# Kernel optimization log

Hardware: AMD Instinct MI355X
Metric: run time of the kernel (lower is better)

## Reference

```python
import jax, jax.numpy as jnp
import numpy as np
from jax import lax

DN = ('NCHW', 'OIHW', 'NCHW')


def _cell(x, h, c, W, b):
    # x,h,c: [B,C,H,W]; W: [4C,2C,3,3]; b: [4C]
    combined = jnp.concatenate([x, h], axis=1)
    y = lax.conv_general_dilated(combined, W, (1, 1), 'SAME', dimension_numbers=DN)
    y = y + b[None, :, None, None]
    cc_i, cc_f, cc_o, cc_g = jnp.split(y, 4, axis=1)
    c_new = jax.nn.sigmoid(cc_f) * c + jax.nn.sigmoid(cc_i) * jnp.tanh(cc_g)
    h_new = jax.nn.sigmoid(cc_o) * jnp.tanh(c_new)
    return h_new, c_new


def _run_level(feats, mask, Wf, bf, Wb, bb):
    # feats: [T,B,C,H,W]; mask: [T,B] int
    zeros = jnp.zeros(feats.shape[1:], feats.dtype)

    def step(carry, xs):
        hf, cf, hb, cb = carry
        x, m = xs
        keep = (m > 0)[:, None, None, None]  # [B,1,1,1]
        nhf, ncf = _cell(x, hf, cf, Wf, bf)
        nhb, ncb = _cell(x, hb, cb, Wb, bb)
        hf = jnp.where(keep, nhf, hf)
        cf = jnp.where(keep, ncf, cf)
        hb = jnp.where(keep, nhb, hb)
        cb = jnp.where(keep, ncb, cb)
        return (hf, cf, hb, cb), None

    (hf, cf, hb, cb), _ = lax.scan(step, (zeros, zeros, zeros, zeros), (feats, mask))
    return (hf + hb) / 2.0


def _make_conv(key, C):
    fan_in = 2 * C * 9
    W = jax.random.normal(key, (4 * C, 2 * C, 3, 3), jnp.float32) / np.sqrt(fan_in)
    b = jnp.zeros((4 * C,), jnp.float32)
    return W, b


def setup_inputs() -> dict:
    key = jax.random.key(0)
    ks = jax.random.split(key, 8)
    feat0 = jax.random.normal(ks[0], (16, 8, 64, 64, 64), jnp.float32)
    feat1 = jax.random.normal(ks[1], (16, 8, 128, 32, 32), jnp.float32)
    mask = jax.random.randint(ks[2], (16, 8), 0, 2, jnp.int32)
    W_fwd0, b_fwd0 = _make_conv(ks[3], 64)
    W_bwd0, b_bwd0 = _make_conv(ks[4], 64)
    W_fwd1, b_fwd1 = _make_conv(ks[5], 128)
    W_bwd1, b_bwd1 = _make_conv(ks[6], 128)
    return {
        'feat0': feat0, 'feat1': feat1, 'mask': mask,
        'W_fwd0': W_fwd0, 'b_fwd0': b_fwd0, 'W_bwd0': W_bwd0, 'b_bwd0': b_bwd0,
        'W_fwd1': W_fwd1, 'b_fwd1': b_fwd1, 'W_bwd1': W_bwd1, 'b_bwd1': b_bwd1,
    }


def reference(feat0, feat1, mask, W_fwd0, b_fwd0, W_bwd0, b_bwd0,
              W_fwd1, b_fwd1, W_bwd1, b_bwd1):
    out0 = _run_level(feat0, mask, W_fwd0, b_fwd0, W_bwd0, b_bwd0)
    out1 = _run_level(feat1, mask, W_fwd1, b_fwd1, W_bwd1, b_bwd1)
    return (out0, out1)
```

## Files before the change

kernel.cpp:

```cpp
#include <hip/hip_runtime.h>

typedef __bf16 bf16x8 __attribute__((ext_vector_type(8)));
typedef float f32x4 __attribute__((ext_vector_type(4)));

__device__ __forceinline__ float sigmoidf_fast(float x) {
  return 1.f / (1.f + __expf(-x));
}
__device__ __forceinline__ float tanhf_fast(float x) {
  float e = __expf(2.f * x);
  return 1.f - 2.f / (e + 1.f);
}
__device__ __forceinline__ unsigned pack2(float a, float b) {
  unsigned short ua = __builtin_bit_cast(unsigned short, (__bf16)a);
  unsigned short ub = __builtin_bit_cast(unsigned short, (__bf16)b);
  return (unsigned)ua | ((unsigned)ub << 16);
}

__global__ void transpose_w_kernel(const float* __restrict__ Wsrc,
                                   __bf16* __restrict__ Wt, int C4, int C2) {
  int idx = blockIdx.x * 256 + threadIdx.x;
  int total = C4 * C2 * 9;
  if (idx >= total) return;
  int SLT = C2 >> 5;
  int j = idx & 7;
  int e = idx >> 3;
  int oc = e % C4; e /= C4;
  int q = e & 3;   e >>= 2;
  int sl = e % SLT;
  int tap = e / SLT;
  int ci = sl * 32 + q * 8 + j;
  Wt[idx] = (__bf16)Wsrc[(oc * C2 + ci) * 9 + tap];
}

__global__ void build_wbuf_kernel(const int* __restrict__ mask,
                                  int* __restrict__ wbuf) {
  int b = threadIdx.x;
  if (b >= 8) return;
  int m = 0;
  for (int t = 0; t < 16; ++t) {
    int w = 0;
    if (mask[t * 8 + b] > 0) { w = m & 1; ++m; }
    wbuf[t * 8 + b] = w;
  }
  wbuf[128 + b] = (m > 0) ? ((m - 1) & 1) : 0;
}

__global__ void combine_kernel(const float* __restrict__ h,
                               const int* __restrict__ fin,
                               float* __restrict__ out, int n, int chw,
                               size_t SZ) {
  int idx = blockIdx.x * 256 + threadIdx.x;
  if (idx >= n) return;
  int b = idx / chw;
  const float* hb = h + (size_t)fin[b] * 2 * SZ;
  out[idx] = (hb[idx] + hb[SZ + idx]) * 0.5f;
}

constexpr int SMEM_BYTES = 107712;

template <int C, int H, int W, int OROWS>
__device__ __forceinline__ void convlstm_block(
    char* smem, const float* __restrict__ x_t,
    const __bf16* __restrict__ Wt, const float* __restrict__ bias,
    const float* __restrict__ h_in, float* __restrict__ h_out,
    float* __restrict__ c_st, int d, int b, int y0, int cs)
{
  constexpr int Bz = 8, C2 = 2 * C, C4 = 4 * C;
  constexpr int COLS = W + 2, C2p = C2 + 8, IMR = OROWS + 2;
  constexpr int PLANE = H * W, CHW = C * PLANE;
  constexpr int SLT = C2 / 32;
  constexpr int LSLT = (SLT == 4) ? 2 : 3;
  constexpr int NSL = 9 * SLT;
  constexpr int ASL = 32 * C4;
  constexpr int CTPR = (W / 16) < 4 ? (W / 16) : 4;
  constexpr int RPG = OROWS / 2;
  constexpr int IMG_ITERS = (C2 / 4) * IMR * W / 512;

  __bf16* sT = (__bf16*)smem;

  const int tid = threadIdx.x;
  const float* hin_b = h_in + (size_t)(d * Bz + b) * CHW;
  float* hout_b = h_out + (size_t)(d * Bz + b) * CHW;
  const __bf16* Wtd = Wt + (size_t)d * (9 * C4 * C2);

  const int lane = tid & 63, wv = tid >> 6;
  const int rg = wv >> 2, wvr = wv & 3;
  const int n = lane & 15, q = lane >> 4;

  const __bf16* Ap = Wtd + (size_t)(q * C4 + cs * 64 + wvr * 16 + n) * 8;

  uint4 A0[4], A1[4];
  auto loadA = [&](int sl, uint4 (&A)[4]) {
    const __bf16* p = Ap + (size_t)sl * ASL;
#pragma unroll
    for (int g = 0; g < 4; ++g)
      A[g] = *reinterpret_cast<const uint4*>(p + g * (C * 8));
  };

  loadA(0, A0);
  loadA(1, A1);

  const float* x_b = x_t + (size_t)b * CHW;
#pragma unroll
  for (int it = 0; it < IMG_ITERS; ++it) {
    int u = it * 512 + tid;
    int x = u % W;
    int t2 = u / W;
    int rr = t2 % IMR, ci4 = t2 / IMR;
    int yy = y0 + rr - 1;
    uint2 pv; pv.x = 0u; pv.y = 0u;
    if (yy >= 0 && yy < H) {
      int ci = ci4 * 4;
      const float* s0 = ((ci < C) ? (x_b + (size_t)ci * PLANE)
                                  : (hin_b + (size_t)(ci - C) * PLANE)) +
                        (size_t)yy * W + x;
      float f0 = s0[0];
      float f1 = s0[PLANE];
      float f2 = s0[2 * PLANE];
      float f3 = s0[3 * PLANE];
      pv.x = pack2(f0, f1);
      pv.y = pack2(f2, f3);
    }
    *reinterpret_cast<uint2*>(&sT[(rr * COLS + x + 1) * C2p + ci4 * 4]) = pv;
  }
  for (int u = tid; u < (C2 / 4) * IMR * 2; u += 512) {
    int ci4 = u / (IMR * 2);
    int rem = u % (IMR * 2);
    int rr = rem >> 1;
    int slot = (rem & 1) ? (W + 1) : 0;
    uint2 z; z.x = 0u; z.y = 0u;
    *reinterpret_cast<uint2*>(&sT[(rr * COLS + slot) * C2p + ci4 * 4]) = z;
  }
  __syncthreads();

  f32x4 acc[4][4];
  f32x4 zero = {0.f, 0.f, 0.f, 0.f};
#pragma unroll
  for (int g = 0; g < 4; ++g)
#pragma unroll
    for (int nt = 0; nt < 4; ++nt) acc[g][nt] = zero;

  auto loadB = [&](int sl, bf16x8 (&Bv)[4]) {
    int tap = sl >> LSLT;
    int ci0 = (sl & (SLT - 1)) * 32;
    int ky = (tap * 11) >> 5;
    int kx = tap - 3 * ky;
#pragma unroll
    for (int nt = 0; nt < 4; ++nt) {
      int row = rg * RPG + nt / CTPR + ky;
      int slot = (nt % CTPR) * 16 + n + kx;
      Bv[nt] = *reinterpret_cast<const bf16x8*>(
          &sT[(row * COLS + slot) * C2p + ci0 + q * 8]);
    }
  };
  auto mfmaAll = [&](uint4 (&A)[4], bf16x8 (&Bv)[4]) {
#pragma unroll
    for (int g = 0; g < 4; ++g) {
      bf16x8 a = __builtin_bit_cast(bf16x8, A[g]);
#pragma unroll
      for (int nt = 0; nt < 4; ++nt)
        acc[g][nt] = __builtin_amdgcn_mfma_f32_16x16x32_bf16(
            a, Bv[nt], acc[g][nt], 0, 0, 0);
    }
  };

  bf16x8 B0[4], B1[4];
  loadB(0, B0);
  loadB(1, B1);
  for (int sl = 0; sl < NSL - 2; sl += 2) {
    mfmaAll(A0, B0);
    loadA(sl + 2, A0);
    loadB(sl + 2, B0);
    mfmaAll(A1, B1);
    loadA(sl + 3, A1);
    loadB(sl + 3, B1);
  }
  mfmaAll(A0, B0);
  mfmaAll(A1, B1);

  float* c_b = c_st + (size_t)(d * Bz + b) * CHW;
#pragma unroll
  for (int r = 0; r < 4; ++r) {
    const int cg = cs * 64 + wvr * 16 + q * 4 + r;
    const float bi = bias[0 * C + cg];
    const float bff = bias[1 * C + cg];
    const float bo = bias[2 * C + cg];
    const float bg = bias[3 * C + cg];
#pragma unroll
    for (int nt = 0; nt < 4; ++nt) {
      const int y = y0 + rg * RPG + nt / CTPR;
      const int x = (nt % CTPR) * 16 + n;
      const size_t off = (size_t)cg * PLANE + (size_t)y * W + x;
      const float vi = acc[0][nt][r] + bi;
      const float vf = acc[1][nt][r] + bff;
      const float vo = acc[2][nt][r] + bo;
      const float vg = acc[3][nt][r] + bg;
      const float cn = sigmoidf_fast(vf) * c_b[off] + sigmoidf_fast(vi) * tanhf_fast(vg);
      c_b[off] = cn;
      hout_b[off] = sigmoidf_fast(vo) * tanhf_fast(cn);
    }
  }
}

__global__ __launch_bounds__(512, 2)
void step_kernel(const float* __restrict__ x0, const float* __restrict__ x1,
                 const int* __restrict__ mask_t, const int* __restrict__ wbuf_t,
                 int* __restrict__ counter,
                 const __bf16* __restrict__ Wt0, const __bf16* __restrict__ Wt1,
                 const float* __restrict__ bf0, const float* __restrict__ bb0,
                 const float* __restrict__ bf1, const float* __restrict__ bb1,
                 float* __restrict__ h0, float* __restrict__ c0,
                 float* __restrict__ h1, float* __restrict__ c1)
{
  __shared__ __align__(16) char smem[SMEM_BYTES];
  __shared__ int s_pop;
  constexpr size_t SZ0 = (size_t)8 * 64 * 64 * 64;
  constexpr size_t SZ1 = (size_t)8 * 128 * 32 * 32;

  for (;;) {
    __syncthreads();
    if (threadIdx.x == 0) s_pop = atomicAdd(counter, 1);
    __syncthreads();
    const int idx = s_pop;
    if (idx >= 768) return;

    if (idx < 256) {
      int grp = idx >> 6;
      int d = grp >> 1, cs = grp & 1;
      int r = idx & 63;
      int b = r & 7, yb = r >> 3;
      if (mask_t[b] <= 0) continue;
      int w = wbuf_t[b];
      convlstm_block<128, 32, 32, 4>(smem, x1, Wt1,
          d == 0 ? bf1 : bb1,
          h1 + (size_t)(1 - w) * 2 * SZ1, h1 + (size_t)w * 2 * SZ1,
          c1, d, b, yb * 4, cs);
    } else {
      int j = idx - 256;
      int d = j >> 8;
      int r = j & 255;
      int b = r & 7, yb = r >> 3;
      if (mask_t[b] <= 0) continue;
      int w = wbuf_t[b];
      convlstm_block<64, 64, 64, 2>(smem, x0, Wt0,
          d == 0 ? bf0 : bb0,
          h0 + (size_t)(1 - w) * 2 * SZ0, h0 + (size_t)w * 2 * SZ0,
          c0, d, b, yb * 2, 0);
    }
  }
}

extern "C" void kernel_launch(void* const* d_in, const int* in_sizes, int n_in,
                              void* d_out, int out_size, void* d_ws, size_t ws_size,
                              hipStream_t stream) {
  const float* feat0 = (const float*)d_in[0];
  const float* feat1 = (const float*)d_in[1];
  const int* mask = (const int*)d_in[2];
  const float* Wf0 = (const float*)d_in[3];
  const float* bf0 = (const float*)d_in[4];
  const float* Wb0 = (const float*)d_in[5];
  const float* bb0 = (const float*)d_in[6];
  const float* Wf1 = (const float*)d_in[7];
  const float* bf1 = (const float*)d_in[8];
  const float* Wb1 = (const float*)d_in[9];
  const float* bb1 = (const float*)d_in[10];

  const int T = 16;
  const size_t SZ0 = (size_t)8 * 64 * 64 * 64;
  const size_t SZ1 = (size_t)8 * 128 * 32 * 32;
  const size_t WT0 = (size_t)9 * 256 * 128;
  const size_t WT1 = (size_t)9 * 512 * 256;

  char* p = (char*)d_ws;
  __bf16* Wt0 = (__bf16*)p; p += 2 * WT0 * sizeof(__bf16);
  __bf16* Wt1 = (__bf16*)p; p += 2 * WT1 * sizeof(__bf16);
  float* h0 = (float*)p;    p += 4 * SZ0 * sizeof(float);
  float* h1 = (float*)p;    p += 4 * SZ1 * sizeof(float);
  float* c0 = (float*)p;    p += 2 * SZ0 * sizeof(float);
  float* c1 = (float*)p;    p += 2 * SZ1 * sizeof(float);
  int* wbuf = (int*)p;      p += 256 * sizeof(int);
  int* counters = (int*)p;  p += 16 * sizeof(int);

  hipMemsetAsync(h0, 0, 4 * SZ0 * sizeof(float), stream);
  hipMemsetAsync(h1, 0, 4 * SZ1 * sizeof(float), stream);
  hipMemsetAsync(c0, 0, 2 * SZ0 * sizeof(float), stream);
  hipMemsetAsync(c1, 0, 2 * SZ1 * sizeof(float), stream);
  hipMemsetAsync(counters, 0, 16 * sizeof(int), stream);

  transpose_w_kernel<<<((int)WT0 + 255) / 256, 256, 0, stream>>>(Wf0, Wt0, 256, 128);
  transpose_w_kernel<<<((int)WT0 + 255) / 256, 256, 0, stream>>>(Wb0, Wt0 + WT0, 256, 128);
  transpose_w_kernel<<<((int)WT1 + 255) / 256, 256, 0, stream>>>(Wf1, Wt1, 512, 256);
  transpose_w_kernel<<<((int)WT1 + 255) / 256, 256, 0, stream>>>(Wb1, Wt1 + WT1, 512, 256);
  build_wbuf_kernel<<<1, 8, 0, stream>>>(mask, wbuf);

  for (int t = 0; t < T; ++t) {
    step_kernel<<<256, 512, 0, stream>>>(
        feat0 + (size_t)t * SZ0, feat1 + (size_t)t * SZ1,
        mask + t * 8, wbuf + t * 8, counters + t,
        Wt0, Wt1, bf0, bb0, bf1, bb1,
        h0, c0, h1, c1);
  }

  float* out = (float*)d_out;
  combine_kernel<<<((int)SZ0 + 255) / 256, 256, 0, stream>>>(
      h0, wbuf + 128, out, (int)SZ0, 64 * 64 * 64, SZ0);
  combine_kernel<<<((int)SZ1 + 255) / 256, 256, 0, stream>>>(
      h1, wbuf + 128, out + SZ0, (int)SZ1, 128 * 32 * 32, SZ1);
}
```

Baseline: 1.297 ms.

## Double per-block output tile and interleave half-tile B loads with MFMAs

```diff
diff --git a/kernel.cpp b/kernel.cpp
--- a/kernel.cpp
+++ b/kernel.cpp
@@ -58,22 +58,24 @@
 
 constexpr int SMEM_BYTES = 107712;
 
-template <int C, int H, int W, int OROWS>
+template <int C, int H, int W, int WAVES_M>
 __device__ __forceinline__ void convlstm_block(
     char* smem, const float* __restrict__ x_t,
     const __bf16* __restrict__ Wt, const float* __restrict__ bias,
     const float* __restrict__ h_in, float* __restrict__ h_out,
-    float* __restrict__ c_st, int d, int b, int y0, int cs)
+    float* __restrict__ c_st, int d, int b, int y0)
 {
   constexpr int Bz = 8, C2 = 2 * C, C4 = 4 * C;
-  constexpr int COLS = W + 2, C2p = C2 + 8, IMR = OROWS + 2;
+  constexpr int OROWS = 4, IMR = OROWS + 2, COLS = W + 2;
+  constexpr int C2p = C2 + 8;
   constexpr int PLANE = H * W, CHW = C * PLANE;
   constexpr int SLT = C2 / 32;
   constexpr int LSLT = (SLT == 4) ? 2 : 3;
   constexpr int NSL = 9 * SLT;
   constexpr int ASL = 32 * C4;
-  constexpr int CTPR = (W / 16) < 4 ? (W / 16) : 4;
-  constexpr int RPG = OROWS / 2;
+  constexpr int RG = 8 / WAVES_M;
+  constexpr int RPG = OROWS / RG;
+  constexpr int CTPR = W / 16;
   constexpr int IMG_ITERS = (C2 / 4) * IMR * W / 512;
 
   __bf16* sT = (__bf16*)smem;
@@ -84,10 +86,11 @@
   const __bf16* Wtd = Wt + (size_t)d * (9 * C4 * C2);
 
   const int lane = tid & 63, wv = tid >> 6;
-  const int rg = wv >> 2, wvr = wv & 3;
+  const int wvm = wv & (WAVES_M - 1);
+  const int rg = wv / WAVES_M;
   const int n = lane & 15, q = lane >> 4;
 
-  const __bf16* Ap = Wtd + (size_t)(q * C4 + cs * 64 + wvr * 16 + n) * 8;
+  const __bf16* Ap = Wtd + (size_t)(q * C4 + wvm * 16 + n) * 8;
 
   uint4 A0[4], A1[4];
   auto loadA = [&](int sl, uint4 (&A)[4]) {
@@ -133,61 +136,63 @@
   }
   __syncthreads();
 
-  f32x4 acc[4][4];
+  f32x4 acc[4][8];
   f32x4 zero = {0.f, 0.f, 0.f, 0.f};
 #pragma unroll
   for (int g = 0; g < 4; ++g)
 #pragma unroll
-    for (int nt = 0; nt < 4; ++nt) acc[g][nt] = zero;
-
-  auto loadB = [&](int sl, bf16x8 (&Bv)[4]) {
+    for (int nt = 0; nt < 8; ++nt) acc[g][nt] = zero;
+
+  auto loadB = [&](int sl, int h, bf16x8 (&Bv)[4]) {
     int tap = sl >> LSLT;
     int ci0 = (sl & (SLT - 1)) * 32;
     int ky = (tap * 11) >> 5;
     int kx = tap - 3 * ky;
 #pragma unroll
-    for (int nt = 0; nt < 4; ++nt) {
+    for (int j = 0; j < 4; ++j) {
+      int nt = h * 4 + j;
       int row = rg * RPG + nt / CTPR + ky;
       int slot = (nt % CTPR) * 16 + n + kx;
-      Bv[nt] = *reinterpret_cast<const bf16x8*>(
+      Bv[j] = *reinterpret_cast<const bf16x8*>(
           &sT[(row * COLS + slot) * C2p + ci0 + q * 8]);
     }
   };
-  auto mfmaAll = [&](uint4 (&A)[4], bf16x8 (&Bv)[4]) {
+  auto mfmaHalf = [&](uint4 (&A)[4], bf16x8 (&Bv)[4], int h) {
 #pragma unroll
     for (int g = 0; g < 4; ++g) {
       bf16x8 a = __builtin_bit_cast(bf16x8, A[g]);
 #pragma unroll
-      for (int nt = 0; nt < 4; ++nt)
-        acc[g][nt] = __builtin_amdgcn_mfma_f32_16x16x32_bf16(
-            a, Bv[nt], acc[g][nt], 0, 0, 0);
+      for (int j = 0; j < 4; ++j)
+        acc[g][h * 4 + j] = __builtin_amdgcn_mfma_f32_16x16x32_bf16(
+            a, Bv[j], acc[g][h * 4 + j], 0, 0, 0);
     }
   };
 
-  bf16x8 B0[4], B1[4];
-  loadB(0, B0);
-  loadB(1, B1);
-  for (int sl = 0; sl < NSL - 2; sl += 2) {
-    mfmaAll(A0, B0);
-    loadA(sl + 2, A0);
-    loadB(sl + 2, B0);
-    mfmaAll(A1, B1);
-    loadA(sl + 3, A1);
-    loadB(sl + 3, B1);
-  }
-  mfmaAll(A0, B0);
-  mfmaAll(A1, B1);
+  bf16x8 Bc[4], Bn[4];
+  loadB(0, 0, Bc);
+  for (int sl = 0; sl < NSL; sl += 2) {
+    loadB(sl, 1, Bn);
+    mfmaHalf(A0, Bc, 0);
+    loadB(sl + 1, 0, Bc);
+    mfmaHalf(A0, Bn, 1);
+    if (sl + 2 < NSL) loadA(sl + 2, A0);
+    loadB(sl + 1, 1, Bn);
+    mfmaHalf(A1, Bc, 0);
+    if (sl + 2 < NSL) loadB(sl + 2, 0, Bc);
+    mfmaHalf(A1, Bn, 1);
+    if (sl + 3 < NSL) loadA(sl + 3, A1);
+  }
 
   float* c_b = c_st + (size_t)(d * Bz + b) * CHW;
 #pragma unroll
   for (int r = 0; r < 4; ++r) {
-    const int cg = cs * 64 + wvr * 16 + q * 4 + r;
+    const int cg = wvm * 16 + q * 4 + r;
     const float bi = bias[0 * C + cg];
     const float bff = bias[1 * C + cg];
     const float bo = bias[2 * C + cg];
     const float bg = bias[3 * C + cg];
 #pragma unroll
-    for (int nt = 0; nt < 4; ++nt) {
+    for (int nt = 0; nt < 8; ++nt) {
       const int y = y0 + rg * RPG + nt / CTPR;
       const int x = (nt % CTPR) * 16 + n;
       const size_t off = (size_t)cg * PLANE + (size_t)y * W + x;
@@ -222,30 +227,29 @@
     if (threadIdx.x == 0) s_pop = atomicAdd(counter, 1);
     __syncthreads();
     const int idx = s_pop;
-    if (idx >= 768) return;
-
-    if (idx < 256) {
-      int grp = idx >> 6;
-      int d = grp >> 1, cs = grp & 1;
+    if (idx >= 384) return;
+
+    if (idx < 128) {
+      int d = idx >> 6;
       int r = idx & 63;
       int b = r & 7, yb = r >> 3;
       if (mask_t[b] <= 0) continue;
       int w = wbuf_t[b];
-      convlstm_block<128, 32, 32, 4>(smem, x1, Wt1,
+      convlstm_block<128, 32, 32, 8>(smem, x1, Wt1,
           d == 0 ? bf1 : bb1,
           h1 + (size_t)(1 - w) * 2 * SZ1, h1 + (size_t)w * 2 * SZ1,
-          c1, d, b, yb * 4, cs);
+          c1, d, b, yb * 4);
     } else {
-      int j = idx - 256;
-      int d = j >> 8;
-      int r = j & 255;
+      int j = idx - 128;
+      int d = j >> 7;
+      int r = j & 127;
       int b = r & 7, yb = r >> 3;
       if (mask_t[b] <= 0) continue;
       int w = wbuf_t[b];
-      convlstm_block<64, 64, 64, 2>(smem, x0, Wt0,
+      convlstm_block<64, 64, 64, 4>(smem, x0, Wt0,
           d == 0 ? bf0 : bb0,
           h0 + (size_t)(1 - w) * 2 * SZ0, h0 + (size_t)w * 2 * SZ0,
-          c0, d, b, yb * 2, 0);
+          c0, d, b, yb * 4);
     }
   }
 }
```

New measurement: 1.938 ms. 49.5% more time.

## Interleave gate weights for contiguous A loads and deepen A prefetch in conv loop

Applied to the files above, without the earlier changes.

```diff
diff --git a/kernel.cpp b/kernel.cpp
--- a/kernel.cpp
+++ b/kernel.cpp
@@ -24,10 +24,13 @@
   int SLT = C2 >> 5;
   int j = idx & 7;
   int e = idx >> 3;
-  int oc = e % C4; e /= C4;
-  int q = e & 3;   e >>= 2;
+  int x = e % C4; e /= C4;
+  int q = e & 3;  e >>= 2;
   int sl = e % SLT;
   int tap = e / SLT;
+  int g = x & 3, ch = x >> 2;
+  int C = C4 >> 2;
+  int oc = g * C + ch;
   int ci = sl * 32 + q * 8 + j;
   Wt[idx] = (__bf16)Wsrc[(oc * C2 + ci) * 9 + tap];
 }
@@ -69,8 +72,6 @@
   constexpr int COLS = W + 2, C2p = C2 + 8, IMR = OROWS + 2;
   constexpr int PLANE = H * W, CHW = C * PLANE;
   constexpr int SLT = C2 / 32;
-  constexpr int LSLT = (SLT == 4) ? 2 : 3;
-  constexpr int NSL = 9 * SLT;
   constexpr int ASL = 32 * C4;
   constexpr int CTPR = (W / 16) < 4 ? (W / 16) : 4;
   constexpr int RPG = OROWS / 2;
@@ -87,18 +88,20 @@
   const int rg = wv >> 2, wvr = wv & 3;
   const int n = lane & 15, q = lane >> 4;
 
-  const __bf16* Ap = Wtd + (size_t)(q * C4 + cs * 64 + wvr * 16 + n) * 8;
-
-  uint4 A0[4], A1[4];
-  auto loadA = [&](int sl, uint4 (&A)[4]) {
-    const __bf16* p = Ap + (size_t)sl * ASL;
+  const __bf16* Ap =
+      Wtd + (size_t)((q * C4 + (cs * 64 + wvr * 16 + n) * 4) * 8);
+
+  uint4 A0[4], A1[4], A2[4], A3[4];
+  auto LD = [&](const __bf16* p, uint4 (&A)[4]) {
 #pragma unroll
     for (int g = 0; g < 4; ++g)
-      A[g] = *reinterpret_cast<const uint4*>(p + g * (C * 8));
+      A[g] = *reinterpret_cast<const uint4*>(p + g * 8);
   };
-
-  loadA(0, A0);
-  loadA(1, A1);
+  LD(Ap, A0);
+  LD(Ap + ASL, A1);
+  LD(Ap + 2 * (size_t)ASL, A2);
+  LD(Ap + 3 * (size_t)ASL, A3);
+  const __bf16* Arun = Ap + 4 * (size_t)ASL;
 
   const float* x_b = x_t + (size_t)b * CHW;
 #pragma unroll
@@ -133,6 +136,14 @@
   }
   __syncthreads();
 
+  const __bf16* Bb[4];
+#pragma unroll
+  for (int nt = 0; nt < 4; ++nt) {
+    int row0 = rg * RPG + nt / CTPR;
+    int slot0 = (nt % CTPR) * 16 + n;
+    Bb[nt] = &sT[(row0 * COLS + slot0) * C2p + q * 8];
+  }
+
   f32x4 acc[4][4];
   f32x4 zero = {0.f, 0.f, 0.f, 0.f};
 #pragma unroll
@@ -140,43 +151,35 @@
 #pragma unroll
     for (int nt = 0; nt < 4; ++nt) acc[g][nt] = zero;
 
-  auto loadB = [&](int sl, bf16x8 (&Bv)[4]) {
-    int tap = sl >> LSLT;
-    int ci0 = (sl & (SLT - 1)) * 32;
+  for (int tap = 0; tap < 9; ++tap) {
     int ky = (tap * 11) >> 5;
     int kx = tap - 3 * ky;
-#pragma unroll
-    for (int nt = 0; nt < 4; ++nt) {
-      int row = rg * RPG + nt / CTPR + ky;
-      int slot = (nt % CTPR) * 16 + n + kx;
-      Bv[nt] = *reinterpret_cast<const bf16x8*>(
-          &sT[(row * COLS + slot) * C2p + ci0 + q * 8]);
+    int toff = (ky * COLS + kx) * C2p;
+    const __bf16* Bt0 = Bb[0] + toff;
+    const __bf16* Bt1 = Bb[1] + toff;
+    const __bf16* Bt2 = Bb[2] + toff;
+    const __bf16* Bt3 = Bb[3] + toff;
+#pragma unroll
+    for (int s = 0; s < SLT; ++s) {
+      bf16x8 b0 = *reinterpret_cast<const bf16x8*>(Bt0 + s * 32);
+      bf16x8 b1 = *reinterpret_cast<const bf16x8*>(Bt1 + s * 32);
+      bf16x8 b2 = *reinterpret_cast<const bf16x8*>(Bt2 + s * 32);
+      bf16x8 b3 = *reinterpret_cast<const bf16x8*>(Bt3 + s * 32);
+      uint4 (&Ac)[4] = (s & 3) == 0 ? A0
+                     : (s & 3) == 1 ? A1
+                     : (s & 3) == 2 ? A2 : A3;
+#pragma unroll
+      for (int g = 0; g < 4; ++g) {
+        bf16x8 a = __builtin_bit_cast(bf16x8, Ac[g]);
+        acc[g][0] = __builtin_amdgcn_mfma_f32_16x16x32_bf16(a, b0, acc[g][0], 0, 0, 0);
+        acc[g][1] = __builtin_amdgcn_mfma_f32_16x16x32_bf16(a, b1, acc[g][1], 0, 0, 0);
+        acc[g][2] = __builtin_amdgcn_mfma_f32_16x16x32_bf16(a, b2, acc[g][2], 0, 0, 0);
+        acc[g][3] = __builtin_amdgcn_mfma_f32_16x16x32_bf16(a, b3, acc[g][3], 0, 0, 0);
+      }
+      LD(Arun, Ac);
+      Arun += ASL;
     }
-  };
-  auto mfmaAll = [&](uint4 (&A)[4], bf16x8 (&Bv)[4]) {
-#pragma unroll
-    for (int g = 0; g < 4; ++g) {
-      bf16x8 a = __builtin_bit_cast(bf16x8, A[g]);
-#pragma unroll
-      for (int nt = 0; nt < 4; ++nt)
-        acc[g][nt] = __builtin_amdgcn_mfma_f32_16x16x32_bf16(
-            a, Bv[nt], acc[g][nt], 0, 0, 0);
-    }
-  };
-
-  bf16x8 B0[4], B1[4];
-  loadB(0, B0);
-  loadB(1, B1);
-  for (int sl = 0; sl < NSL - 2; sl += 2) {
-    mfmaAll(A0, B0);
-    loadA(sl + 2, A0);
-    loadB(sl + 2, B0);
-    mfmaAll(A1, B1);
-    loadA(sl + 3, A1);
-    loadB(sl + 3, B1);
-  }
-  mfmaAll(A0, B0);
-  mfmaAll(A1, B1);
+  }
 
   float* c_b = c_st + (size_t)(d * Bz + b) * CHW;
 #pragma unroll
@@ -270,10 +273,11 @@
   const size_t SZ1 = (size_t)8 * 128 * 32 * 32;
   const size_t WT0 = (size_t)9 * 256 * 128;
   const size_t WT1 = (size_t)9 * 512 * 256;
+  const size_t APAD = (size_t)4 * 32 * 512;
 
   char* p = (char*)d_ws;
   __bf16* Wt0 = (__bf16*)p; p += 2 * WT0 * sizeof(__bf16);
-  __bf16* Wt1 = (__bf16*)p; p += 2 * WT1 * sizeof(__bf16);
+  __bf16* Wt1 = (__bf16*)p; p += (2 * WT1 + APAD) * sizeof(__bf16);
   float* h0 = (float*)p;    p += 4 * SZ0 * sizeof(float);
   float* h1 = (float*)p;    p += 4 * SZ1 * sizeof(float);
   float* c0 = (float*)p;    p += 2 * SZ0 * sizeof(float);
```

Result: slower. 1.617 ms (+24.7%).
